# Optimization experiments

Hardware: AMD Instinct MI355X
Metric: run time of the kernel (lower is better)

Reference implementation:

```python
import jax, jax.numpy as jnp
import numpy as np

N = 524288      # total nodes across batched subgraphs
E = 4194304     # total edges (avg degree ~8)
B = 4096        # number of subgraphs (links)
H = 32          # hidden_dim
L = 3           # num_layers
K = 30          # sort-pool k
MAXZ = 1000     # max DRNL label
EPS = 1e-5      # BatchNorm eps


def setup_inputs() -> dict:
    key = jax.random.key(0)
    ks = jax.random.split(key, 12)
    x_z = jax.random.randint(ks[0], (N,), 0, MAXZ + 1, dtype=jnp.int32)
    edge_index = jax.random.randint(ks[1], (2, E), 0, N, dtype=jnp.int32)
    batch = jnp.sort(jax.random.randint(ks[2], (N,), 0, B, dtype=jnp.int32))
    # parameters
    emb = jax.random.normal(ks[3], (MAXZ + 1, H), jnp.float32) * 0.1
    Wc = jax.random.normal(ks[4], (L, H, H), jnp.float32) * (1.0 / np.sqrt(H))
    bc = jnp.zeros((L, H), jnp.float32)
    gamma = jnp.ones((L, H), jnp.float32)
    beta = jnp.zeros((L, H), jnp.float32)
    rmean = jax.random.normal(ks[5], (L, H), jnp.float32) * 0.1
    rvar = 1.0 + 0.1 * jax.random.uniform(ks[6], (L, H), jnp.float32)
    W1 = jax.random.normal(ks[7], (K * H, H), jnp.float32) * (1.0 / np.sqrt(K * H))
    b1 = jnp.zeros((H,), jnp.float32)
    W2 = jax.random.normal(ks[8], (H, H // 2), jnp.float32) * (1.0 / np.sqrt(H))
    b2 = jnp.zeros((H // 2,), jnp.float32)
    W3 = jax.random.normal(ks[9], (H // 2, 1), jnp.float32) * (1.0 / np.sqrt(H // 2))
    b3 = jnp.zeros((1,), jnp.float32)
    return dict(x_z=x_z, edge_index=edge_index, batch=batch, emb=emb, Wc=Wc, bc=bc,
                gamma=gamma, beta=beta, rmean=rmean, rvar=rvar,
                W1=W1, b1=b1, W2=W2, b2=b2, W3=W3, b3=b3)


def reference(x_z, edge_index, batch, emb, Wc, bc, gamma, beta, rmean, rvar,
              W1, b1, W2, b2, W3, b3):
    src, dst = edge_index[0], edge_index[1]
    # GCN symmetric normalization with added self-loops: deg[i] = in_deg(i) + 1
    deg = jnp.zeros((N,), jnp.float32).at[dst].add(1.0) + 1.0
    dinv = jax.lax.rsqrt(deg)
    enorm = dinv[src] * dinv[dst]          # [E]
    self_norm = dinv * dinv                # [N] self-loop coefficient

    x = emb[x_z]                           # [N, H]
    for i in range(L):
        h = x @ Wc[i]                      # [N, H]
        agg = (jnp.zeros_like(h).at[dst].add(h[src] * enorm[:, None])
               + h * self_norm[:, None] + bc[i])
        # BatchNorm1d (eval: running stats) + ReLU; dropout is identity in eval
        xn = (agg - rmean[i]) * jax.lax.rsqrt(rvar[i] + EPS) * gamma[i] + beta[i]
        x = jax.nn.relu(xn)

    # SortAggregation: per-graph sort desc by last channel, keep top-K, zero-pad
    order = jnp.lexsort((-x[:, -1], batch))   # group by graph, desc by last feat
    xs = x[order]
    bs = batch[order]
    counts = jnp.zeros((B,), jnp.int32).at[batch].add(1)
    starts = jnp.concatenate([jnp.zeros((1,), jnp.int32), jnp.cumsum(counts)[:-1]])
    rank = jnp.arange(N, dtype=jnp.int32) - starts[bs]
    slot = jnp.where(rank < K, rank, K)       # overflow -> dummy slot K
    pooled = jnp.zeros((B, K + 1, H), x.dtype).at[bs, slot].set(xs)
    pooled = pooled[:, :K].reshape(B, K * H)  # [B, K*H]

    h1 = jax.nn.relu(pooled @ W1 + b1)
    h2 = jax.nn.relu(h1 @ W2 + b2)
    out = (h2 @ W3 + b3)[:, 0]                # [B]
    return out
```

## Files before the change

kernel.cpp:

```cpp
#include <hip/hip_runtime.h>
#include <hip/hip_bf16.h>
#include <stdint.h>

#define N_NODES 524288
#define N_EDGES 4194304
#define N_GRAPHS 4096
#define HDIM 32
#define NLAYERS 3
#define KPOOL 30
#define MAXC 1024

#define NBUCKET 1024
#define BSHIFT 9
#define NPB 512
#define NCOPY 8
#define HIST_SZ (NBUCKET * NCOPY)

__global__ void k_hist(const int* __restrict__ dst, int* __restrict__ ghist) {
    __shared__ int lh[NBUCKET];
    int t = threadIdx.x;
    for (int i = t; i < NBUCKET; i += 256) lh[i] = 0;
    __syncthreads();
    int base = blockIdx.x * 2048;
    for (int i = t; i < 2048; i += 256) {
        int d = dst[base + i];
        atomicAdd(&lh[d >> BSHIFT], 1);
    }
    __syncthreads();
    int c = blockIdx.x & 7;
    for (int i = t; i < NBUCKET; i += 256) {
        int v = lh[i];
        if (v) atomicAdd(&ghist[i * NCOPY + c], v);
    }
}

__global__ void k_scan8k(const int* __restrict__ ghist, int* __restrict__ gbase,
                         int* __restrict__ cur) {
    __shared__ int tmp[256];
    int t = threadIdx.x;
    int loc[32];
    int s = 0;
    for (int k = 0; k < 32; ++k) { loc[k] = ghist[t * 32 + k]; s += loc[k]; }
    tmp[t] = s;
    __syncthreads();
    for (int d = 1; d < 256; d <<= 1) {
        int a = (t >= d) ? tmp[t - d] : 0;
        __syncthreads();
        tmp[t] += a;
        __syncthreads();
    }
    int run = tmp[t] - s;
    for (int k = 0; k < 32; ++k) {
        gbase[t * 32 + k] = run;
        cur[t * 32 + k] = run;
        run += loc[k];
    }
}

__global__ void k_bin(const int* __restrict__ src, const int* __restrict__ dst,
                      int* __restrict__ cur, unsigned long long* __restrict__ stage) {
    int base = blockIdx.x * 2048;
    int c = blockIdx.x & 7;
    int t = threadIdx.x;
    for (int i = t; i < 2048; i += 256) {
        int e = base + i;
        int d = dst[e];
        int b = d >> BSHIFT;
        int pos = atomicAdd(&cur[b * NCOPY + c], 1);
        unsigned long long rec = ((unsigned long long)(unsigned)src[e] << 32)
                               | (unsigned)((e << BSHIFT) | (d & (NPB - 1)));
        stage[pos] = rec;
    }
}

__global__ void k_build(const unsigned long long* __restrict__ stage,
                        const int* __restrict__ gbase,
                        float* __restrict__ dinv, int* __restrict__ offs,
                        unsigned long long* __restrict__ csr2) {
    __shared__ int cnt[NPB];
    __shared__ int sstart[NPB];
    __shared__ int tmp[256];
    int b = blockIdx.x, t = threadIdx.x;
    int s0 = gbase[b * NCOPY];
    int s1 = (b == NBUCKET - 1) ? N_EDGES : gbase[(b + 1) * NCOPY];
    for (int j = t; j < NPB; j += 256) cnt[j] = 0;
    __syncthreads();
    for (int i = s0 + t; i < s1; i += 256) {
        unsigned key = (unsigned)stage[i];
        atomicAdd(&cnt[key & (NPB - 1)], 1);
    }
    __syncthreads();
    int j0 = 2 * t, j1 = 2 * t + 1;
    int a0 = cnt[j0], a1 = cnt[j1];
    {
        float d0 = (float)(a0 + 1);
        float q0 = (float)sqrt((double)d0);
        dinv[b * NPB + j0] = (float)(1.0 / (double)q0);
        float d1 = (float)(a1 + 1);
        float q1 = (float)sqrt((double)d1);
        dinv[b * NPB + j1] = (float)(1.0 / (double)q1);
    }
    int s = a0 + a1;
    tmp[t] = s;
    __syncthreads();
    for (int d = 1; d < 256; d <<= 1) {
        int a = (t >= d) ? tmp[t - d] : 0;
        __syncthreads();
        tmp[t] += a;
        __syncthreads();
    }
    int run = tmp[t] - s;
    sstart[j0] = run;
    sstart[j1] = run + a0;
    offs[b * NPB + j0] = s0 + run;
    offs[b * NPB + j1] = s0 + run + a0;
    if (b == NBUCKET - 1 && t == 255) offs[N_NODES] = N_EDGES;
    cnt[j0] = run;
    cnt[j1] = run + a0;
    __syncthreads();
    for (int i = s0 + t; i < s1; i += 256) {
        unsigned long long v = stage[i];
        int pos = s0 + atomicAdd(&cnt[(unsigned)v & (NPB - 1)], 1);
        csr2[pos] = v;
    }
    __syncthreads();
    for (int jj = 0; jj < 2; ++jj) {
        int j = 2 * t + jj;
        int beg = s0 + sstart[j];
        int end = s0 + cnt[j];
        for (int i = beg + 1; i < end; ++i) {
            unsigned long long v = csr2[i];
            unsigned kv = (unsigned)v;
            int q = i - 1;
            while (q >= beg && (unsigned)csr2[q] > kv) { csr2[q + 1] = csr2[q]; --q; }
            csr2[q + 1] = v;
        }
    }
}

__global__ void k_pack(const float* __restrict__ dinv, unsigned long long* __restrict__ csr2) {
    int i = blockIdx.x * 256 + threadIdx.x;
    if (i < N_EDGES) {
        unsigned long long r = csr2[i];
        int s = (int)(r >> 32);
        csr2[i] = (r & 0xffffffff00000000ull) | (unsigned)__float_as_uint(dinv[s]);
    }
}

__global__ void k_bnprep(const float* __restrict__ rvar, float* __restrict__ rs) {
    int i = threadIdx.x;
    if (i < NLAYERS * HDIM) {
        float rv = __fadd_rn(rvar[i], 1e-5f);
        float sq = (float)sqrt((double)rv);
        rs[i] = (float)(1.0 / (double)sq);
    }
}

__global__ void k_embed_mm(const int* __restrict__ xz, const float* __restrict__ emb,
                           const float* __restrict__ Wc, float* __restrict__ h) {
    __shared__ float Wl[HDIM * HDIM];
    __shared__ float xt[256];
    int t = threadIdx.x;
    int base = blockIdx.x * 256;
    for (int i = t; i < HDIM * HDIM; i += 256) Wl[i] = Wc[i];
    {
        int gid = base + t;
        int n = gid >> 5, c = gid & 31;
        xt[t] = emb[xz[n] * HDIM + c];
    }
    __syncthreads();
    int nl = t >> 5, c = t & 31;
    float acc = 0.0f;
#pragma unroll
    for (int k = 0; k < HDIM; ++k) acc = __fmaf_rn(xt[nl * HDIM + k], Wl[k * HDIM + c], acc);
    h[base + t] = acc;
}

__device__ __forceinline__ float agg_phase(const float* __restrict__ h,
                                           const float* __restrict__ dinv,
                                           const int* __restrict__ offs,
                                           const unsigned long long* __restrict__ csr2,
                                           const float* __restrict__ bc,
                                           const float* __restrict__ rmean,
                                           const float* __restrict__ rs,
                                           const float* __restrict__ gamma,
                                           const float* __restrict__ beta,
                                           int gid) {
    int n = gid >> 5, c = gid & 31;
    float di = dinv[n];
    float hself = h[gid];
    float accE = 0.0f;
    int beg = offs[n], end = offs[n + 1];
    int i = beg;
    for (; i + 8 <= end; i += 8) {
        unsigned long long r0 = csr2[i];
        unsigned long long r1 = csr2[i + 1];
        unsigned long long r2 = csr2[i + 2];
        unsigned long long r3 = csr2[i + 3];
        unsigned long long r4 = csr2[i + 4];
        unsigned long long r5 = csr2[i + 5];
        unsigned long long r6 = csr2[i + 6];
        unsigned long long r7 = csr2[i + 7];
        float h0 = h[(int)(r0 >> 32) * HDIM + c];
        float h1 = h[(int)(r1 >> 32) * HDIM + c];
        float h2 = h[(int)(r2 >> 32) * HDIM + c];
        float h3 = h[(int)(r3 >> 32) * HDIM + c];
        float h4 = h[(int)(r4 >> 32) * HDIM + c];
        float h5 = h[(int)(r5 >> 32) * HDIM + c];
        float h6 = h[(int)(r6 >> 32) * HDIM + c];
        float h7 = h[(int)(r7 >> 32) * HDIM + c];
        accE = __fadd_rn(accE, __fmul_rn(h0, __fmul_rn(__uint_as_float((unsigned)r0), di)));
        accE = __fadd_rn(accE, __fmul_rn(h1, __fmul_rn(__uint_as_float((unsigned)r1), di)));
        accE = __fadd_rn(accE, __fmul_rn(h2, __fmul_rn(__uint_as_float((unsigned)r2), di)));
        accE = __fadd_rn(accE, __fmul_rn(h3, __fmul_rn(__uint_as_float((unsigned)r3), di)));
        accE = __fadd_rn(accE, __fmul_rn(h4, __fmul_rn(__uint_as_float((unsigned)r4), di)));
        accE = __fadd_rn(accE, __fmul_rn(h5, __fmul_rn(__uint_as_float((unsigned)r5), di)));
        accE = __fadd_rn(accE, __fmul_rn(h6, __fmul_rn(__uint_as_float((unsigned)r6), di)));
        accE = __fadd_rn(accE, __fmul_rn(h7, __fmul_rn(__uint_as_float((unsigned)r7), di)));
    }
    for (; i + 4 <= end; i += 4) {
        unsigned long long r0 = csr2[i];
        unsigned long long r1 = csr2[i + 1];
        unsigned long long r2 = csr2[i + 2];
        unsigned long long r3 = csr2[i + 3];
        float h0 = h[(int)(r0 >> 32) * HDIM + c];
        float h1 = h[(int)(r1 >> 32) * HDIM + c];
        float h2 = h[(int)(r2 >> 32) * HDIM + c];
        float h3 = h[(int)(r3 >> 32) * HDIM + c];
        accE = __fadd_rn(accE, __fmul_rn(h0, __fmul_rn(__uint_as_float((unsigned)r0), di)));
        accE = __fadd_rn(accE, __fmul_rn(h1, __fmul_rn(__uint_as_float((unsigned)r1), di)));
        accE = __fadd_rn(accE, __fmul_rn(h2, __fmul_rn(__uint_as_float((unsigned)r2), di)));
        accE = __fadd_rn(accE, __fmul_rn(h3, __fmul_rn(__uint_as_float((unsigned)r3), di)));
    }
    for (; i < end; ++i) {
        unsigned long long r = csr2[i];
        float hv = h[(int)(r >> 32) * HDIM + c];
        float dv = __uint_as_float((unsigned)r);
        accE = __fadd_rn(accE, __fmul_rn(hv, __fmul_rn(dv, di)));
    }
    float sn = __fmul_rn(di, di);
    float t1 = __fmul_rn(hself, sn);
    float a2 = __fadd_rn(accE, t1);
    float a3 = __fadd_rn(a2, bc[c]);
    float tt = __fsub_rn(a3, rmean[c]);
    float u  = __fmul_rn(tt, rs[c]);
    float v  = __fmul_rn(u, gamma[c]);
    float xn = __fadd_rn(v, beta[c]);
    return (xn > 0.0f) ? xn : 0.0f;
}

__global__ void k_agg_mm(const float* __restrict__ h, const float* __restrict__ dinv,
                         const int* __restrict__ offs,
                         const unsigned long long* __restrict__ csr2,
                         const float* __restrict__ bc, const float* __restrict__ rmean,
                         const float* __restrict__ rs, const float* __restrict__ gamma,
                         const float* __restrict__ beta,
                         const float* __restrict__ Wnext, float* __restrict__ hout) {
    __shared__ float Wl[HDIM * HDIM];
    __shared__ float xt[256];
    int t = threadIdx.x;
    int base = blockIdx.x * 256;
    for (int i = t; i < HDIM * HDIM; i += 256) Wl[i] = Wnext[i];
    xt[t] = agg_phase(h, dinv, offs, csr2, bc, rmean, rs, gamma, beta, base + t);
    __syncthreads();
    int nl = t >> 5, c = t & 31;
    float acc = 0.0f;
#pragma unroll
    for (int k = 0; k < HDIM; ++k) acc = __fmaf_rn(xt[nl * HDIM + k], Wl[k * HDIM + c], acc);
    hout[base + t] = acc;
}

__global__ void k_agg_last(const float* __restrict__ h, const float* __restrict__ dinv,
                           const int* __restrict__ offs,
                           const unsigned long long* __restrict__ csr2,
                           const float* __restrict__ bc, const float* __restrict__ rmean,
                           const float* __restrict__ rs, const float* __restrict__ gamma,
                           const float* __restrict__ beta, float* __restrict__ xout,
                           float* __restrict__ lastc) {
    int gid = blockIdx.x * 256 + threadIdx.x;
    float v = agg_phase(h, dinv, offs, csr2, bc, rmean, rs, gamma, beta, gid);
    xout[gid] = v;
    if ((gid & 31) == 31) lastc[gid >> 5] = v;
}

__global__ void k_starts(const int* __restrict__ batch, int* __restrict__ start) {
    int n = blockIdx.x * 256 + threadIdx.x;
    if (n >= N_NODES) return;
    int bn = batch[n];
    int bp = (n == 0) ? -1 : batch[n - 1];
    for (int g = bp + 1; g <= bn; ++g) start[g] = n;
    if (n == N_NODES - 1) {
        for (int g = bn + 1; g <= N_GRAPHS; ++g) start[g] = N_NODES;
    }
}

__global__ void k_pool_mlp(const float* __restrict__ x, const float* __restrict__ lastc,
                           const int* __restrict__ start,
                           const float* __restrict__ W1, const float* __restrict__ b1,
                           const float* __restrict__ W2, const float* __restrict__ b2,
                           const float* __restrict__ W3, const float* __restrict__ b3,
                           float* __restrict__ out) {
    int g = blockIdx.x;
    int t = threadIdx.x;
    int s = start[g], e = start[g + 1];
    int cnt = e - s;

    __shared__ unsigned long long keys[MAXC];
    __shared__ int sel[KPOOL];
    __shared__ float pl[KPOOL * HDIM];
    __shared__ double part[64];
    __shared__ double h1[HDIM];
    __shared__ double h2[HDIM / 2];

    bool inlds = (cnt <= MAXC);
    if (inlds) {
        for (int i = t; i < cnt; i += 64) {
            int n = s + i;
            keys[i] = ((unsigned long long)__float_as_uint(lastc[n]) << 32)
                    | (unsigned int)(~n);
        }
    }
    __syncthreads();

    unsigned long long prev = ~0ull;
    for (int k = 0; k < KPOOL; ++k) {
        if (k < cnt) {
            unsigned long long best = 0ull;
            if (inlds) {
                for (int i = t; i < cnt; i += 64) {
                    unsigned long long key = keys[i];
                    if (key < prev && key > best) best = key;
                }
            } else {
                for (int n = s + t; n < e; n += 64) {
                    unsigned long long key =
                        ((unsigned long long)__float_as_uint(lastc[n]) << 32)
                        | (unsigned int)(~n);
                    if (key < prev && key > best) best = key;
                }
            }
            for (int off = 32; off; off >>= 1) {
                unsigned long long o = __shfl_down(best, off);
                if (o > best) best = o;
            }
            best = __shfl(best, 0);
            prev = best;
            if (t == 0) sel[k] = (int)(~((unsigned int)(best & 0xffffffffull)));
        } else {
            if (t == 0) sel[k] = -1;
        }
    }
    __syncthreads();

    for (int idx = t; idx < KPOOL * HDIM; idx += 64) {
        int k = idx >> 5, c = idx & 31;
        int n = sel[k];
        pl[idx] = (n >= 0) ? x[n * HDIM + c] : 0.0f;
    }
    __syncthreads();

    {
        int j = t & 31;
        int half = t >> 5;
        double acc = 0.0;
        int r0 = half * (KPOOL * HDIM / 2);
        for (int r = r0; r < r0 + KPOOL * HDIM / 2; ++r)
            acc += (double)pl[r] * (double)W1[r * HDIM + j];
        part[t] = acc;
    }
    __syncthreads();
    if (t < HDIM) {
        double v = part[t] + part[t + 32] + (double)b1[t];
        h1[t] = (v > 0.0) ? v : 0.0;
    }
    __syncthreads();

    if (t < HDIM / 2) {
        double a2 = (double)b2[t];
        for (int i = 0; i < HDIM; ++i) a2 += h1[i] * (double)W2[i * (HDIM / 2) + t];
        h2[t] = (a2 > 0.0) ? a2 : 0.0;
    }
    __syncthreads();

    if (t == 0) {
        double o = (double)b3[0];
        for (int i = 0; i < HDIM / 2; ++i) o += h2[i] * (double)W3[i];
        out[g] = (float)o;
    }
}

extern "C" void kernel_launch(void* const* d_in, const int* in_sizes, int n_in,
                              void* d_out, int out_size, void* d_ws, size_t ws_size,
                              hipStream_t stream) {
    const int*   xz    = (const int*)d_in[0];
    const int*   src   = (const int*)d_in[1];
    const int*   dst   = (const int*)d_in[1] + N_EDGES;
    const int*   batch = (const int*)d_in[2];
    const float* emb   = (const float*)d_in[3];
    const float* Wc    = (const float*)d_in[4];
    const float* bc    = (const float*)d_in[5];
    const float* gamma = (const float*)d_in[6];
    const float* beta  = (const float*)d_in[7];
    const float* rmean = (const float*)d_in[8];
    const float* rvar  = (const float*)d_in[9];
    const float* W1    = (const float*)d_in[10];
    const float* b1    = (const float*)d_in[11];
    const float* W2    = (const float*)d_in[12];
    const float* b2    = (const float*)d_in[13];
    const float* W3    = (const float*)d_in[14];
    const float* b3    = (const float*)d_in[15];
    float* out = (float*)d_out;

    char* p = (char*)d_ws;
    auto carve = [&](size_t bytes) {
        void* q = (void*)p;
        p += (bytes + 255) & ~size_t(255);
        return q;
    };
    int*   ghist = (int*)carve(HIST_SZ * 4);
    int*   gbase = (int*)carve(HIST_SZ * 4);
    int*   cur   = (int*)carve(HIST_SZ * 4);
    unsigned long long* stage = (unsigned long long*)carve((size_t)N_EDGES * 8);
    unsigned long long* csr2  = (unsigned long long*)carve((size_t)N_EDGES * 8);
    float* dinv  = (float*)carve(N_NODES * 4);
    int*   offs  = (int*)carve((N_NODES + 1) * 4);
    int*   start = (int*)carve((N_GRAPHS + 1) * 4);
    float* rs    = (float*)carve(NLAYERS * HDIM * 4);
    float* lastc = (float*)carve(N_NODES * 4);
    float* bufA  = (float*)carve((size_t)N_NODES * HDIM * 4);
    float* bufB  = (float*)carve((size_t)N_NODES * HDIM * 4);

    hipMemsetAsync(ghist, 0, HIST_SZ * 4, stream);

    k_hist<<<N_EDGES / 2048, 256, 0, stream>>>(dst, ghist);
    k_scan8k<<<1, 256, 0, stream>>>(ghist, gbase, cur);
    k_bin<<<N_EDGES / 2048, 256, 0, stream>>>(src, dst, cur, stage);
    k_build<<<NBUCKET, 256, 0, stream>>>(stage, gbase, dinv, offs, csr2);
    k_pack<<<N_EDGES / 256, 256, 0, stream>>>(dinv, csr2);
    k_bnprep<<<1, 128, 0, stream>>>(rvar, rs);
    k_starts<<<N_NODES / 256, 256, 0, stream>>>(batch, start);

    const int NG = (N_NODES * HDIM) / 256;
    k_embed_mm<<<NG, 256, 0, stream>>>(xz, emb, Wc + 0 * HDIM * HDIM, bufA);
    k_agg_mm<<<NG, 256, 0, stream>>>(bufA, dinv, offs, csr2,
        bc + 0 * HDIM, rmean + 0 * HDIM, rs + 0 * HDIM, gamma + 0 * HDIM, beta + 0 * HDIM,
        Wc + 1 * HDIM * HDIM, bufB);
    k_agg_mm<<<NG, 256, 0, stream>>>(bufB, dinv, offs, csr2,
        bc + 1 * HDIM, rmean + 1 * HDIM, rs + 1 * HDIM, gamma + 1 * HDIM, beta + 1 * HDIM,
        Wc + 2 * HDIM * HDIM, bufA);
    k_agg_last<<<NG, 256, 0, stream>>>(bufA, dinv, offs, csr2,
        bc + 2 * HDIM, rmean + 2 * HDIM, rs + 2 * HDIM, gamma + 2 * HDIM, beta + 2 * HDIM,
        bufB, lastc);

    k_pool_mlp<<<N_GRAPHS, 64, 0, stream>>>(bufB, lastc, start, W1, b1, W2, b2, W3, b3, out);
}
```

Baseline: 1.212 ms.

## Build CSR in LDS with fused dinv packing and degree-sorted node permutation

Node degrees are now computed in the histogram pass, with a separate dinv kernel, so dinv can be packed into edge records while the CSR is built, removing the k_pack pass. Each bucket is scattered and insertion-sorted in shared memory when it fits, instead of in global memory. A per-bucket permutation sorts nodes by in-degree, and the aggregation kernels process nodes in that order so wavefronts see similar edge counts and diverge less. The cost is a global atomic per edge for degrees, an O(512^2) rank computation per bucket, and uncoalesced hout writes through the permutation.

Result: slower. 1.277 ms (+5.4%).

```diff
diff --git a/kernel.cpp b/kernel.cpp
--- a/kernel.cpp
+++ b/kernel.cpp
@@ -15,8 +15,12 @@
 #define NPB 512
 #define NCOPY 8
 #define HIST_SZ (NBUCKET * NCOPY)
-
-__global__ void k_hist(const int* __restrict__ dst, int* __restrict__ ghist) {
+#define CAP 6144
+
+typedef unsigned long long ull;
+
+__global__ void k_hist(const int* __restrict__ dst, int* __restrict__ ghist,
+                       int* __restrict__ deg) {
     __shared__ int lh[NBUCKET];
     int t = threadIdx.x;
     for (int i = t; i < NBUCKET; i += 256) lh[i] = 0;
@@ -25,12 +29,22 @@
     for (int i = t; i < 2048; i += 256) {
         int d = dst[base + i];
         atomicAdd(&lh[d >> BSHIFT], 1);
+        atomicAdd(&deg[d], 1);
     }
     __syncthreads();
     int c = blockIdx.x & 7;
     for (int i = t; i < NBUCKET; i += 256) {
         int v = lh[i];
         if (v) atomicAdd(&ghist[i * NCOPY + c], v);
+    }
+}
+
+__global__ void k_dinv(const int* __restrict__ deg, float* __restrict__ dinv) {
+    int n = blockIdx.x * 256 + threadIdx.x;
+    if (n < N_NODES) {
+        float d = (float)(deg[n] + 1);
+        float sq = (float)sqrt((double)d);
+        dinv[n] = (float)(1.0 / (double)sq);
     }
 }
 
@@ -58,7 +72,7 @@
 }
 
 __global__ void k_bin(const int* __restrict__ src, const int* __restrict__ dst,
-                      int* __restrict__ cur, unsigned long long* __restrict__ stage) {
+                      int* __restrict__ cur, ull* __restrict__ stage) {
     int base = blockIdx.x * 2048;
     int c = blockIdx.x & 7;
     int t = threadIdx.x;
@@ -67,39 +81,35 @@
         int d = dst[e];
         int b = d >> BSHIFT;
         int pos = atomicAdd(&cur[b * NCOPY + c], 1);
-        unsigned long long rec = ((unsigned long long)(unsigned)src[e] << 32)
-                               | (unsigned)((e << BSHIFT) | (d & (NPB - 1)));
+        ull rec = ((ull)(unsigned)src[e] << 32)
+                | (unsigned)(((d & (NPB - 1)) << 22) | e);
         stage[pos] = rec;
     }
 }
 
-__global__ void k_build(const unsigned long long* __restrict__ stage,
-                        const int* __restrict__ gbase,
-                        float* __restrict__ dinv, int* __restrict__ offs,
-                        unsigned long long* __restrict__ csr2) {
+__global__ void k_build(const ull* __restrict__ stage, const int* __restrict__ gbase,
+                        const float* __restrict__ dinv,
+                        int* __restrict__ offs, ull* __restrict__ csr2,
+                        int* __restrict__ perm) {
+    __shared__ ull grp[CAP];
     __shared__ int cnt[NPB];
     __shared__ int sstart[NPB];
+    __shared__ int cur[NPB];
     __shared__ int tmp[256];
     int b = blockIdx.x, t = threadIdx.x;
     int s0 = gbase[b * NCOPY];
     int s1 = (b == NBUCKET - 1) ? N_EDGES : gbase[(b + 1) * NCOPY];
+    int win = s1 - s0;
     for (int j = t; j < NPB; j += 256) cnt[j] = 0;
     __syncthreads();
-    for (int i = s0 + t; i < s1; i += 256) {
-        unsigned key = (unsigned)stage[i];
-        atomicAdd(&cnt[key & (NPB - 1)], 1);
+    const unsigned* lo32 = (const unsigned*)stage;
+    for (int i = t; i < win; i += 256) {
+        unsigned k = lo32[2 * (s0 + i)];
+        atomicAdd(&cnt[(k >> 22) & (NPB - 1)], 1);
     }
     __syncthreads();
     int j0 = 2 * t, j1 = 2 * t + 1;
     int a0 = cnt[j0], a1 = cnt[j1];
-    {
-        float d0 = (float)(a0 + 1);
-        float q0 = (float)sqrt((double)d0);
-        dinv[b * NPB + j0] = (float)(1.0 / (double)q0);
-        float d1 = (float)(a1 + 1);
-        float q1 = (float)sqrt((double)d1);
-        dinv[b * NPB + j1] = (float)(1.0 / (double)q1);
-    }
     int s = a0 + a1;
     tmp[t] = s;
     __syncthreads();
@@ -110,40 +120,86 @@
         __syncthreads();
     }
     int run = tmp[t] - s;
-    sstart[j0] = run;
-    sstart[j1] = run + a0;
+    sstart[j0] = run;      sstart[j1] = run + a0;
+    cur[j0] = run;         cur[j1] = run + a0;
     offs[b * NPB + j0] = s0 + run;
     offs[b * NPB + j1] = s0 + run + a0;
     if (b == NBUCKET - 1 && t == 255) offs[N_NODES] = N_EDGES;
-    cnt[j0] = run;
-    cnt[j1] = run + a0;
-    __syncthreads();
-    for (int i = s0 + t; i < s1; i += 256) {
-        unsigned long long v = stage[i];
-        int pos = s0 + atomicAdd(&cnt[(unsigned)v & (NPB - 1)], 1);
-        csr2[pos] = v;
+    __syncthreads();
+
+    if (win <= CAP) {
+        for (int i = t; i < win; i += 256) {
+            ull v = stage[s0 + i];
+            unsigned k = (unsigned)v;
+            int pos = atomicAdd(&cur[(k >> 22) & (NPB - 1)], 1);
+            grp[pos] = v;
+        }
+        __syncthreads();
+        for (int jj = 0; jj < 2; ++jj) {
+            int j = 2 * t + jj;
+            int beg = sstart[j], end = beg + cnt[j];
+            for (int i = beg + 1; i < end; ++i) {
+                ull v = grp[i];
+                unsigned kv = (unsigned)v;
+                int q = i - 1;
+                while (q >= beg && (unsigned)grp[q] > kv) { grp[q + 1] = grp[q]; --q; }
+                grp[q + 1] = v;
+            }
+        }
+        __syncthreads();
+        int i = t;
+        for (; i + 768 < win; i += 1024) {
+            ull v0 = grp[i], v1 = grp[i + 256], v2 = grp[i + 512], v3 = grp[i + 768];
+            float d0 = dinv[(int)(v0 >> 32)];
+            float d1 = dinv[(int)(v1 >> 32)];
+            float d2 = dinv[(int)(v2 >> 32)];
+            float d3 = dinv[(int)(v3 >> 32)];
+            csr2[s0 + i]       = (v0 & 0xffffffff00000000ull) | (unsigned)__float_as_uint(d0);
+            csr2[s0 + i + 256] = (v1 & 0xffffffff00000000ull) | (unsigned)__float_as_uint(d1);
+            csr2[s0 + i + 512] = (v2 & 0xffffffff00000000ull) | (unsigned)__float_as_uint(d2);
+            csr2[s0 + i + 768] = (v3 & 0xffffffff00000000ull) | (unsigned)__float_as_uint(d3);
+        }
+        for (; i < win; i += 256) {
+            ull v = grp[i];
+            float dv = dinv[(int)(v >> 32)];
+            csr2[s0 + i] = (v & 0xffffffff00000000ull) | (unsigned)__float_as_uint(dv);
+        }
+    } else {
+        for (int i = t; i < win; i += 256) {
+            ull v = stage[s0 + i];
+            unsigned k = (unsigned)v;
+            int pos = s0 + atomicAdd(&cur[(k >> 22) & (NPB - 1)], 1);
+            csr2[pos] = v;
+        }
+        __syncthreads();
+        for (int jj = 0; jj < 2; ++jj) {
+            int j = 2 * t + jj;
+            int beg = s0 + sstart[j], end = beg + cnt[j];
+            for (int i = beg + 1; i < end; ++i) {
+                ull v = csr2[i];
+                unsigned kv = (unsigned)v;
+                int q = i - 1;
+                while (q >= beg && (unsigned)csr2[q] > kv) { csr2[q + 1] = csr2[q]; --q; }
+                csr2[q + 1] = v;
+            }
+        }
+        __syncthreads();
+        for (int i = t; i < win; i += 256) {
+            ull v = csr2[s0 + i];
+            float dv = dinv[(int)(v >> 32)];
+            csr2[s0 + i] = (v & 0xffffffff00000000ull) | (unsigned)__float_as_uint(dv);
+        }
     }
     __syncthreads();
     for (int jj = 0; jj < 2; ++jj) {
         int j = 2 * t + jj;
-        int beg = s0 + sstart[j];
-        int end = s0 + cnt[j];
-        for (int i = beg + 1; i < end; ++i) {
-            unsigned long long v = csr2[i];
-            unsigned kv = (unsigned)v;
-            int q = i - 1;
-            while (q >= beg && (unsigned)csr2[q] > kv) { csr2[q + 1] = csr2[q]; --q; }
-            csr2[q + 1] = v;
-        }
-    }
-}
-
-__global__ void k_pack(const float* __restrict__ dinv, unsigned long long* __restrict__ csr2) {
-    int i = blockIdx.x * 256 + threadIdx.x;
-    if (i < N_EDGES) {
-        unsigned long long r = csr2[i];
-        int s = (int)(r >> 32);
-        csr2[i] = (r & 0xffffffff00000000ull) | (unsigned)__float_as_uint(dinv[s]);
+        int dj = cnt[j];
+        int r = 0;
+        for (int k = 0; k < NPB; ++k) {
+            int dk = cnt[k];
+            r += (dk < dj) || (dk == dj && k < j);
+        }
+        perm[b * NPB + r] = b * NPB + j;
     }
 }
 
@@ -179,28 +235,27 @@
 __device__ __forceinline__ float agg_phase(const float* __restrict__ h,
                                            const float* __restrict__ dinv,
                                            const int* __restrict__ offs,
-                                           const unsigned long long* __restrict__ csr2,
+                                           const ull* __restrict__ csr2,
                                            const float* __restrict__ bc,
                                            const float* __restrict__ rmean,
                                            const float* __restrict__ rs,
                                            const float* __restrict__ gamma,
                                            const float* __restrict__ beta,
-                                           int gid) {
-    int n = gid >> 5, c = gid & 31;
+                                           int n, int c) {
     float di = dinv[n];
-    float hself = h[gid];
+    float hself = h[n * HDIM + c];
     float accE = 0.0f;
     int beg = offs[n], end = offs[n + 1];
     int i = beg;
     for (; i + 8 <= end; i += 8) {
-        unsigned long long r0 = csr2[i];
-        unsigned long long r1 = csr2[i + 1];
-        unsigned long long r2 = csr2[i + 2];
-        unsigned long long r3 = csr2[i + 3];
-        unsigned long long r4 = csr2[i + 4];
-        unsigned long long r5 = csr2[i + 5];
-        unsigned long long r6 = csr2[i + 6];
-        unsigned long long r7 = csr2[i + 7];
+        ull r0 = csr2[i];
+        ull r1 = csr2[i + 1];
+        ull r2 = csr2[i + 2];
+        ull r3 = csr2[i + 3];
+        ull r4 = csr2[i + 4];
+        ull r5 = csr2[i + 5];
+        ull r6 = csr2[i + 6];
+        ull r7 = csr2[i + 7];
         float h0 = h[(int)(r0 >> 32) * HDIM + c];
         float h1 = h[(int)(r1 >> 32) * HDIM + c];
         float h2 = h[(int)(r2 >> 32) * HDIM + c];
@@ -219,10 +274,10 @@
         accE = __fadd_rn(accE, __fmul_rn(h7, __fmul_rn(__uint_as_float((unsigned)r7), di)));
     }
     for (; i + 4 <= end; i += 4) {
-        unsigned long long r0 = csr2[i];
-        unsigned long long r1 = csr2[i + 1];
-        unsigned long long r2 = csr2[i + 2];
-        unsigned long long r3 = csr2[i + 3];
+        ull r0 = csr2[i];
+        ull r1 = csr2[i + 1];
+        ull r2 = csr2[i + 2];
+        ull r3 = csr2[i + 3];
         float h0 = h[(int)(r0 >> 32) * HDIM + c];
         float h1 = h[(int)(r1 >> 32) * HDIM + c];
         float h2 = h[(int)(r2 >> 32) * HDIM + c];
@@ -233,7 +288,7 @@
         accE = __fadd_rn(accE, __fmul_rn(h3, __fmul_rn(__uint_as_float((unsigned)r3), di)));
     }
     for (; i < end; ++i) {
-        unsigned long long r = csr2[i];
+        ull r = csr2[i];
         float hv = h[(int)(r >> 32) * HDIM + c];
         float dv = __uint_as_float((unsigned)r);
         accE = __fadd_rn(accE, __fmul_rn(hv, __fmul_rn(dv, di)));
@@ -250,37 +305,45 @@
 }
 
 __global__ void k_agg_mm(const float* __restrict__ h, const float* __restrict__ dinv,
-                         const int* __restrict__ offs,
-                         const unsigned long long* __restrict__ csr2,
+                         const int* __restrict__ offs, const ull* __restrict__ csr2,
+                         const int* __restrict__ perm,
                          const float* __restrict__ bc, const float* __restrict__ rmean,
                          const float* __restrict__ rs, const float* __restrict__ gamma,
                          const float* __restrict__ beta,
                          const float* __restrict__ Wnext, float* __restrict__ hout) {
     __shared__ float Wl[HDIM * HDIM];
     __shared__ float xt[256];
-    int t = threadIdx.x;
-    int base = blockIdx.x * 256;
+    __shared__ int nodes[8];
+    int t = threadIdx.x;
     for (int i = t; i < HDIM * HDIM; i += 256) Wl[i] = Wnext[i];
-    xt[t] = agg_phase(h, dinv, offs, csr2, bc, rmean, rs, gamma, beta, base + t);
-    __syncthreads();
-    int nl = t >> 5, c = t & 31;
+    if (t < 8) nodes[t] = perm[blockIdx.x * 8 + t];
+    __syncthreads();
+    int slot = t >> 5, c = t & 31;
+    int n = nodes[slot];
+    xt[t] = agg_phase(h, dinv, offs, csr2, bc, rmean, rs, gamma, beta, n, c);
+    __syncthreads();
     float acc = 0.0f;
 #pragma unroll
-    for (int k = 0; k < HDIM; ++k) acc = __fmaf_rn(xt[nl * HDIM + k], Wl[k * HDIM + c], acc);
-    hout[base + t] = acc;
+    for (int k = 0; k < HDIM; ++k) acc = __fmaf_rn(xt[slot * HDIM + k], Wl[k * HDIM + c], acc);
+    hout[n * HDIM + c] = acc;
 }
 
 __global__ void k_agg_last(const float* __restrict__ h, const float* __restrict__ dinv,
-                           const int* __restrict__ offs,
-                           const unsigned long long* __restrict__ csr2,
+                           const int* __restrict__ offs, const ull* __restrict__ csr2,
+                           const int* __restrict__ perm,
                            const float* __restrict__ bc, const float* __restrict__ rmean,
                            const float* __restrict__ rs, const float* __restrict__ gamma,
                            const float* __restrict__ beta, float* __restrict__ xout,
                            float* __restrict__ lastc) {
-    int gid = blockIdx.x * 256 + threadIdx.x;
-    float v = agg_phase(h, dinv, offs, csr2, bc, rmean, rs, gamma, beta, gid);
-    xout[gid] = v;
-    if ((gid & 31) == 31) lastc[gid >> 5] = v;
+    __shared__ int nodes[8];
+    int t = threadIdx.x;
+    if (t < 8) nodes[t] = perm[blockIdx.x * 8 + t];
+    __syncthreads();
+    int slot = t >> 5, c = t & 31;
+    int n = nodes[slot];
+    float v = agg_phase(h, dinv, offs, csr2, bc, rmean, rs, gamma, beta, n, c);
+    xout[n * HDIM + c] = v;
+    if (c == 31) lastc[n] = v;
 }
 
 __global__ void k_starts(const int* __restrict__ batch, int* __restrict__ start) {
@@ -305,7 +368,7 @@
     int s = start[g], e = start[g + 1];
     int cnt = e - s;
 
-    __shared__ unsigned long long keys[MAXC];
+    __shared__ ull keys[MAXC];
     __shared__ int sel[KPOOL];
     __shared__ float pl[KPOOL * HDIM];
     __shared__ double part[64];
@@ -316,31 +379,28 @@
     if (inlds) {
         for (int i = t; i < cnt; i += 64) {
             int n = s + i;
-            keys[i] = ((unsigned long long)__float_as_uint(lastc[n]) << 32)
-                    | (unsigned int)(~n);
-        }
-    }
-    __syncthreads();
-
-    unsigned long long prev = ~0ull;
+            keys[i] = ((ull)__float_as_uint(lastc[n]) << 32) | (unsigned int)(~n);
+        }
+    }
+    __syncthreads();
+
+    ull prev = ~0ull;
     for (int k = 0; k < KPOOL; ++k) {
         if (k < cnt) {
-            unsigned long long best = 0ull;
+            ull best = 0ull;
             if (inlds) {
                 for (int i = t; i < cnt; i += 64) {
-                    unsigned long long key = keys[i];
+                    ull key = keys[i];
                     if (key < prev && key > best) best = key;
                 }
             } else {
                 for (int n = s + t; n < e; n += 64) {
-                    unsigned long long key =
-                        ((unsigned long long)__float_as_uint(lastc[n]) << 32)
-                        | (unsigned int)(~n);
+                    ull key = ((ull)__float_as_uint(lastc[n]) << 32) | (unsigned int)(~n);
                     if (key < prev && key > best) best = key;
                 }
             }
             for (int off = 32; off; off >>= 1) {
-                unsigned long long o = __shfl_down(best, off);
+                ull o = __shfl_down(best, off);
                 if (o > best) best = o;
             }
             best = __shfl(best, 0);
@@ -420,10 +480,12 @@
     int*   ghist = (int*)carve(HIST_SZ * 4);
     int*   gbase = (int*)carve(HIST_SZ * 4);
     int*   cur   = (int*)carve(HIST_SZ * 4);
-    unsigned long long* stage = (unsigned long long*)carve((size_t)N_EDGES * 8);
-    unsigned long long* csr2  = (unsigned long long*)carve((size_t)N_EDGES * 8);
+    int*   deg   = (int*)carve(N_NODES * 4);
+    ull*   stage = (ull*)carve((size_t)N_EDGES * 8);
+    ull*   csr2  = (ull*)carve((size_t)N_EDGES * 8);
     float* dinv  = (float*)carve(N_NODES * 4);
     int*   offs  = (int*)carve((N_NODES + 1) * 4);
+    int*   permB = (int*)carve(N_NODES * 4);
     int*   start = (int*)carve((N_GRAPHS + 1) * 4);
     float* rs    = (float*)carve(NLAYERS * HDIM * 4);
     float* lastc = (float*)carve(N_NODES * 4);
@@ -431,24 +493,25 @@
     float* bufB  = (float*)carve((size_t)N_NODES * HDIM * 4);
 
     hipMemsetAsync(ghist, 0, HIST_SZ * 4, stream);
-
-    k_hist<<<N_EDGES / 2048, 256, 0, stream>>>(dst, ghist);
+    hipMemsetAsync(deg, 0, N_NODES * 4, stream);
+
+    k_hist<<<N_EDGES / 2048, 256, 0, stream>>>(dst, ghist, deg);
     k_scan8k<<<1, 256, 0, stream>>>(ghist, gbase, cur);
+    k_dinv<<<N_NODES / 256, 256, 0, stream>>>(deg, dinv);
     k_bin<<<N_EDGES / 2048, 256, 0, stream>>>(src, dst, cur, stage);
-    k_build<<<NBUCKET, 256, 0, stream>>>(stage, gbase, dinv, offs, csr2);
-    k_pack<<<N_EDGES / 256, 256, 0, stream>>>(dinv, csr2);
+    k_build<<<NBUCKET, 256, 0, stream>>>(stage, gbase, dinv, offs, csr2, permB);
     k_bnprep<<<1, 128, 0, stream>>>(rvar, rs);
     k_starts<<<N_NODES / 256, 256, 0, stream>>>(batch, start);
 
     const int NG = (N_NODES * HDIM) / 256;
     k_embed_mm<<<NG, 256, 0, stream>>>(xz, emb, Wc + 0 * HDIM * HDIM, bufA);
-    k_agg_mm<<<NG, 256, 0, stream>>>(bufA, dinv, offs, csr2,
+    k_agg_mm<<<N_NODES / 8, 256, 0, stream>>>(bufA, dinv, offs, csr2, permB,
         bc + 0 * HDIM, rmean + 0 * HDIM, rs + 0 * HDIM, gamma + 0 * HDIM, beta + 0 * HDIM,
         Wc + 1 * HDIM * HDIM, bufB);
-    k_agg_mm<<<NG, 256, 0, stream>>>(bufB, dinv, offs, csr2,
+    k_agg_mm<<<N_NODES / 8, 256, 0, stream>>>(bufB, dinv, offs, csr2, permB,
         bc + 1 * HDIM, rmean + 1 * HDIM, rs + 1 * HDIM, gamma + 1 * HDIM, beta + 1 * HDIM,
         Wc + 2 * HDIM * HDIM, bufA);
-    k_agg_last<<<NG, 256, 0, stream>>>(bufA, dinv, offs, csr2,
+    k_agg_last<<<N_NODES / 8, 256, 0, stream>>>(bufA, dinv, offs, csr2, permB,
         bc + 2 * HDIM, rmean + 2 * HDIM, rs + 2 * HDIM, gamma + 2 * HDIM, beta + 2 * HDIM,
         bufB, lastc);
 
```
